# Optimization experiments

Measured on AMD Instinct MI355X. Metric: run time of the kernel, lower is better.

## Reference

```python
import jax, jax.numpy as jnp
import numpy as np

HEADS = 32
K_TOP = 512  # top-k tokens gathered from KV


def conv3d(x, w, b=None, pad=0, groups=1):
    # x: [B,C,D,H,W], w: [O, I/groups, kd,kh,kw]
    out = jax.lax.conv_general_dilated(
        x, w, window_strides=(1, 1, 1), padding=[(pad, pad)] * 3,
        dimension_numbers=("NCDHW", "OIDHW", "NCDHW"), feature_group_count=groups)
    if b is not None:
        out = out + b[None, :, None, None, None]
    return out


def setup_inputs() -> dict:
    key = jax.random.key(0)
    ks = jax.random.split(key, 10)
    B, C, D, H, W = 2, 256, 16, 16, 16
    p = lambda i, shape: (jax.random.normal(ks[i], shape, jnp.float32) * 0.02)
    return {
        "x_kv": jax.random.normal(ks[0], (B, C, D, H, W), jnp.float32),
        "x_q": jax.random.normal(ks[1], (B, C, D, H, W), jnp.float32),
        "w_spa": p(2, (1, 2, 7, 7, 7)),            # SpatialAttention conv, no bias
        "w_kv": p(3, (C, 2 * C)), "b_kv": jnp.zeros((2 * C,), jnp.float32),
        "w_q": p(4, (C, C)), "b_q": jnp.zeros((C,), jnp.float32),
        "w_proj": p(5, (C, C)), "b_proj": jnp.zeros((C,), jnp.float32),
        "w_dw": p(6, (C, 1, 3, 3, 3)), "b_dw": jnp.zeros((C,), jnp.float32),  # depthwise 3x3x3
        "w_pw": p(7, (C, C, 1, 1, 1)), "b_pw": jnp.zeros((C,), jnp.float32),  # pointwise 1x1x1
    }


def reference(x_kv, x_q, w_spa, w_kv, b_kv, w_q, b_q, w_proj, b_proj,
              w_dw, b_dw, w_pw, b_pw):
    B, C, D, H, W = x_kv.shape
    N = D * H * W
    hd = C // HEADS
    scale = hd ** -0.5

    # SpatialAttention: channel mean/max -> conv(2->1, k=7, pad=3) -> sigmoid
    avg = jnp.mean(x_kv, axis=1, keepdims=True)
    mx = jnp.max(x_kv, axis=1, keepdims=True)
    spa = jax.nn.sigmoid(conv3d(jnp.concatenate([avg, mx], axis=1), w_spa, None, pad=3))
    scores = spa.reshape(B, N)                      # [B, N]
    _, idx = jax.lax.top_k(scores, K_TOP)           # [B, K] (descending, like torch.topk)

    # Full K/V projection over all N tokens (as in original), then gather top-k
    xkv_t = x_kv.reshape(B, C, N).transpose(0, 2, 1)        # [B, N, C]
    kv = xkv_t @ w_kv + b_kv                                 # [B, N, 2C]
    k_full, v_full = kv[..., :C], kv[..., C:]
    k_g = jnp.take_along_axis(k_full, idx[:, :, None], axis=1)  # [B, K, C]
    v_g = jnp.take_along_axis(v_full, idx[:, :, None], axis=1)
    k_g = k_g.reshape(B, K_TOP, HEADS, hd).transpose(0, 2, 1, 3)  # [B, h, K, d]
    v_g = v_g.reshape(B, K_TOP, HEADS, hd).transpose(0, 2, 1, 3)

    # Queries over all Nq tokens
    xq_t = x_q.reshape(B, C, N).transpose(0, 2, 1)           # [B, N, C]
    q = (xq_t @ w_q + b_q).reshape(B, N, HEADS, hd).transpose(0, 2, 1, 3)  # [B, h, N, d]

    attn = jax.nn.softmax(jnp.einsum('bhnd,bhkd->bhnk', q, k_g) * scale, axis=-1)
    out = jnp.einsum('bhnk,bhkd->bhnd', attn, v_g)           # [B, h, N, d]
    out = out.transpose(0, 2, 1, 3).reshape(B, N, C)
    out = out @ w_proj + b_proj
    out = out.transpose(0, 2, 1).reshape(B, C, D, H, W)

    # DWconv residual on full (ungathered) V
    v_vol = v_full.transpose(0, 2, 1).reshape(B, C, D, H, W)
    res = conv3d(conv3d(v_vol, w_dw, b_dw, pad=1, groups=C), w_pw, b_pw)
    return out + res
```

## Files before the change

### kernel.cpp

```cpp
#include <hip/hip_runtime.h>
#include <hip/hip_bf16.h>

typedef short bf16x8 __attribute__((ext_vector_type(8)));
typedef float f32x4 __attribute__((ext_vector_type(4)));

constexpr int CN = 256, NV = 4096, KTOP = 512;

static __device__ __forceinline__ unsigned short f2bf(float f) {
  __hip_bfloat16 h = __float2bfloat16(f);
  return *(unsigned short*)&h;
}
static __device__ __forceinline__ unsigned pack2(float a, float b) {
  return (unsigned)f2bf(a) | ((unsigned)f2bf(b) << 16);
}
static __device__ __forceinline__ float bf2f(unsigned short u) {
  return __uint_as_float(((unsigned)u) << 16);
}
static __device__ __forceinline__ unsigned packtrunc(float a, float b) {
  return (__float_as_uint(a) >> 16) | (__float_as_uint(b) & 0xFFFF0000u);
}

__global__ void __launch_bounds__(256) k_stage1(const float* __restrict__ xkv,
                                                const float* __restrict__ xq,
                                                const float* __restrict__ wkv,
                                                const float* __restrict__ wq,
                                                const float* __restrict__ wproj,
                                                const float* __restrict__ wpw,
                                                unsigned short* __restrict__ xkv_t,
                                                unsigned short* __restrict__ xq_t,
                                                float* __restrict__ avgmx,
                                                unsigned short* __restrict__ wv_t,
                                                unsigned short* __restrict__ wq_t,
                                                unsigned short* __restrict__ wcat,
                                                unsigned short* __restrict__ wk_t) {
  __shared__ float tile[64 * 65];
  int z = blockIdx.z;
  int t = threadIdx.x;
  if (z == 4) {
    __shared__ float ssum[256], smax[256];
    int blk = blockIdx.y * 64 + blockIdx.x;
    int b = blk >> 7, n0 = (blk & 127) * 32;
    int cg = t >> 5, nl = t & 31;
    int n = n0 + nl;
    const float* p = xkv + (size_t)b * CN * NV + (size_t)cg * 32 * NV + n;
    float s = 0.f, m = -1e30f;
    for (int i = 0; i < 32; ++i) {
      float v = p[(size_t)i * NV];
      s += v; m = fmaxf(m, v);
    }
    ssum[t] = s; smax[t] = m;
    __syncthreads();
    if (cg == 0) {
      for (int g = 1; g < 8; ++g) { s += ssum[g * 32 + nl]; m = fmaxf(m, smax[g * 32 + nl]); }
      avgmx[(b * 2 + 0) * NV + n] = s * (1.0f / 256.0f);
      avgmx[(b * 2 + 1) * NV + n] = m;
    }
    return;
  }
  if (z >= 5) {
    if (blockIdx.x >= 4 || blockIdx.y >= 4) return;
    int role = z - 5;
    int j0 = blockIdx.x * 64, c0 = blockIdx.y * 64;
    if (role == 3) {
      int j = t >> 2, part = t & 3;
      const float* s = &wpw[(size_t)(j0 + j) * 256 + c0 + part * 16];
      unsigned w[8];
#pragma unroll
      for (int k = 0; k < 8; ++k) w[k] = pack2(s[2 * k], s[2 * k + 1]);
      uint4* p = (uint4*)&wcat[(size_t)(j0 + j) * 512 + 256 + c0 + part * 16];
      p[0] = make_uint4(w[0], w[1], w[2], w[3]);
      p[1] = make_uint4(w[4], w[5], w[6], w[7]);
      return;
    }
    const float* src; int srcLD, srcOff; unsigned short* dst; int dstLD;
    if (role == 0)      { src = wkv;   srcLD = 512; srcOff = 256; dst = wv_t; dstLD = 256; }
    else if (role == 1) { src = wq;    srcLD = 256; srcOff = 0;   dst = wq_t; dstLD = 256; }
    else if (role == 4) { src = wkv;   srcLD = 512; srcOff = 0;   dst = wk_t; dstLD = 256; }
    else                { src = wproj; srcLD = 256; srcOff = 0;   dst = wcat; dstLD = 512; }
    for (int i = 0; i < 16; ++i) {
      int id = i * 256 + t, c = id >> 6, j = id & 63;
      tile[c * 65 + j] = src[(size_t)(c0 + c) * srcLD + srcOff + j0 + j];
    }
    __syncthreads();
    int j = t & 63, part = t >> 6;
    unsigned w[8];
#pragma unroll
    for (int k = 0; k < 8; ++k)
      w[k] = pack2(tile[(part * 16 + 2 * k) * 65 + j], tile[(part * 16 + 2 * k + 1) * 65 + j]);
    uint4* p = (uint4*)&dst[(size_t)(j0 + j) * dstLD + c0 + part * 16];
    p[0] = make_uint4(w[0], w[1], w[2], w[3]);
    p[1] = make_uint4(w[4], w[5], w[6], w[7]);
    return;
  }
  int b = z & 1;
  const float* s = (z < 2 ? xkv : xq) + (size_t)b * CN * NV;
  unsigned short* d = (z < 2 ? xkv_t : xq_t) + (size_t)b * NV * 256;
  int c0 = blockIdx.y * 64, n0 = blockIdx.x * 64;
  for (int i = 0; i < 16; ++i) {
    int id = i * 256 + t, c = id >> 6, n = id & 63;
    tile[c * 65 + n] = s[(size_t)(c0 + c) * NV + n0 + n];
  }
  __syncthreads();
  int n = t & 63, part = t >> 6;
  unsigned w[8];
#pragma unroll
  for (int k = 0; k < 8; ++k)
    w[k] = pack2(tile[(part * 16 + 2 * k) * 65 + n], tile[(part * 16 + 2 * k + 1) * 65 + n]);
  uint4* p = (uint4*)&d[(size_t)(n0 + n) * 256 + c0 + part * 16];
  p[0] = make_uint4(w[0], w[1], w[2], w[3]);
  p[1] = make_uint4(w[4], w[5], w[6], w[7]);
}

__global__ void __launch_bounds__(256) k_stage2(const unsigned short* __restrict__ xkv_t,
                                                const unsigned short* __restrict__ xq_t,
                                                const unsigned short* __restrict__ wv_t,
                                                const unsigned short* __restrict__ wq_t,
                                                const float* __restrict__ bkv,
                                                const float* __restrict__ bq,
                                                const float* __restrict__ avgmx,
                                                const float* __restrict__ wspa,
                                                unsigned short* __restrict__ v_nc,
                                                unsigned short* __restrict__ qh,
                                                float* __restrict__ scores) {
  __shared__ alignas(16) char smem[35520];
  int z = blockIdx.z;
  int t = threadIdx.x;
  if (z == 4) {
    float* vol = (float*)smem;
    float* ws = (float*)(smem + 32768);
    int id = blockIdx.y * 32 + blockIdx.x;
    int b = id >> 5, chunk = id & 31;
    for (int i = t; i < 8192; i += 256) vol[i] = avgmx[b * 8192 + i];
    for (int i = t; i < 686; i += 256) ws[i] = wspa[i];
    __syncthreads();
    int ci = t & 1;
    int n = chunk * 128 + (t >> 1);
    int d = n >> 8, h = (n >> 4) & 15, w = n & 15;
    const float* vb = vol + ci * 4096;
    const float* wb = ws + ci * 343;
    float acc = 0.f;
    for (int kd = 0; kd < 7; ++kd) {
      int zd = d - 3 + kd; if ((unsigned)zd >= 16u) continue;
      for (int kh = 0; kh < 7; ++kh) {
        int zh = h - 3 + kh; if ((unsigned)zh >= 16u) continue;
        const float* row = vb + zd * 256 + zh * 16;
        const float* wr = wb + kd * 49 + kh * 7;
#pragma unroll
        for (int kw = 0; kw < 7; ++kw) {
          int zw = w - 3 + kw;
          if ((unsigned)zw < 16u) acc += row[zw] * wr[kw];
        }
      }
    }
    acc += __shfl_xor(acc, 1);
    if (ci == 0) scores[b * NV + n] = 1.0f / (1.0f + expf(-acc));
    return;
  }
  unsigned short* Als = (unsigned short*)smem;
  unsigned short* Bls = Als + 128 * 40;
  int role = z;
  int b = role & 1;
  bool isQ = role >= 2;
  const unsigned short* A = isQ ? wq_t : wv_t;
  const unsigned short* B = (isQ ? xq_t : xkv_t) + (size_t)b * NV * 256;
  const float* bias = isQ ? bq : (bkv + 256);
  int n0 = blockIdx.x * 128, j0 = blockIdx.y * 128;
  int wave = t >> 6, lane = t & 63;
  int l15 = lane & 15, q = lane >> 4, q8 = q * 8;
  int wj = (wave >> 1) * 64, wn = (wave & 1) * 64;
  f32x4 acc[4][4] = {};
  int ar = t >> 1, ah = t & 1;
  for (int c0 = 0; c0 < 256; c0 += 32) {
    __syncthreads();
    {
      const unsigned short* sa = &A[(size_t)(j0 + ar) * 256 + c0 + ah * 16];
      *(uint4*)&Als[ar * 40 + ah * 16]     = *(const uint4*)&sa[0];
      *(uint4*)&Als[ar * 40 + ah * 16 + 8] = *(const uint4*)&sa[8];
      const unsigned short* sb = &B[(size_t)(n0 + ar) * 256 + c0 + ah * 16];
      *(uint4*)&Bls[ar * 40 + ah * 16]     = *(const uint4*)&sb[0];
      *(uint4*)&Bls[ar * 40 + ah * 16 + 8] = *(const uint4*)&sb[8];
    }
    __syncthreads();
    bf16x8 af[4], bf[4];
#pragma unroll
    for (int mt = 0; mt < 4; ++mt)
      af[mt] = *(const bf16x8*)&Als[(wj + mt * 16 + l15) * 40 + q8];
#pragma unroll
    for (int nt = 0; nt < 4; ++nt)
      bf[nt] = *(const bf16x8*)&Bls[(wn + nt * 16 + l15) * 40 + q8];
#pragma unroll
    for (int mt = 0; mt < 4; ++mt)
#pragma unroll
      for (int nt = 0; nt < 4; ++nt)
        acc[mt][nt] = __builtin_amdgcn_mfma_f32_16x16x32_bf16(af[mt], bf[nt], acc[mt][nt], 0, 0, 0);
  }
#pragma unroll
  for (int mt = 0; mt < 4; ++mt) {
    int jb = j0 + wj + mt * 16 + q * 4;
    float4 b4 = *(const float4*)&bias[jb];
#pragma unroll
    for (int nt = 0; nt < 4; ++nt) {
      int n = n0 + wn + nt * 16 + l15;
      float v0 = acc[mt][nt][0] + b4.x;
      float v1 = acc[mt][nt][1] + b4.y;
      float v2 = acc[mt][nt][2] + b4.z;
      float v3 = acc[mt][nt][3] + b4.w;
      uint2 pk = make_uint2(pack2(v0, v1), pack2(v2, v3));
      if (isQ) {
        int h = jb >> 3, d0 = jb & 7;
        *(uint2*)&qh[((size_t)(b * 32 + h) * NV + n) * 8 + d0] = pk;
      } else {
        *(uint2*)&v_nc[((size_t)b * NV + n) * 256 + jb] = pk;
      }
    }
  }
}

__global__ void __launch_bounds__(1024) k_stage3(const float* __restrict__ scores,
                                                 int* __restrict__ idx,
                                                 const unsigned short* __restrict__ v_nc,
                                                 const float* __restrict__ wdw,
                                                 const float* __restrict__ bdw,
                                                 unsigned short* __restrict__ aoydw) {
  int b = blockIdx.z;
  int bx = blockIdx.x;
  int tid = threadIdx.x;
  if (bx == 256) {
    __shared__ unsigned sv[4096];
    __shared__ int sB;
    __shared__ unsigned sSub, scnt;
    __shared__ unsigned hist[256];
    __shared__ int wsum[16];
    for (int t = tid; t < 4096; t += 1024) sv[t] = __float_as_uint(scores[b * NV + t]);
    if (tid == 0) scnt = 0;
    unsigned prefix = 0;
    int r = 512;
    for (int shift = 24; shift >= 0; shift -= 8) {
      if (tid < 256) hist[tid] = 0;
      __syncthreads();
      unsigned maskhi = (shift == 24) ? 0u : (0xFFFFFFFFu << (shift + 8));
      for (int i = 0; i < 4; ++i) {
        unsigned v = sv[tid + i * 1024];
        if ((v & maskhi) == prefix) atomicAdd(&hist[(v >> shift) & 255], 1u);
      }
      __syncthreads();
      if (tid < 64) {
        int lane = tid;
        unsigned h0 = hist[lane * 4 + 0], h1 = hist[lane * 4 + 1];
        unsigned h2 = hist[lane * 4 + 2], h3 = hist[lane * 4 + 3];
        unsigned s = h0 + h1 + h2 + h3;
        for (int off = 1; off < 64; off <<= 1) {
          unsigned y = __shfl_down(s, off);
          if (lane + off < 64) s += y;
        }
        unsigned tail = __shfl_down(s, 1);
        if (lane == 63) tail = 0;
        unsigned s3 = tail + h3, s2 = s3 + h2, s1 = s2 + h1, s0 = s1 + h0;
        unsigned sx[5] = {s0, s1, s2, s3, tail};
#pragma unroll
        for (int i = 0; i < 4; ++i)
          if (sx[i] >= (unsigned)r && sx[i + 1] < (unsigned)r) { sB = lane * 4 + i; sSub = sx[i + 1]; }
      }
      __syncthreads();
      prefix |= ((unsigned)sB) << shift;
      r -= (int)sSub;
      __syncthreads();
    }
    unsigned vstar = prefix;
    for (int i = 0; i < 4; ++i) {
      int t = tid * 4 + i;
      if (sv[t] > vstar) { unsigned p = atomicAdd(&scnt, 1u); idx[b * KTOP + p] = t; }
    }
    __syncthreads();
    int base = (int)scnt;
    int loc = 0;
    for (int i = 0; i < 4; ++i) loc += (sv[tid * 4 + i] == vstar);
    int lane = tid & 63, w = tid >> 6;
    int x = loc;
    for (int off = 1; off < 64; off <<= 1) {
      int y = __shfl_up(x, off);
      if (lane >= off) x += y;
    }
    if (lane == 63) wsum[w] = x;
    __syncthreads();
    int wbase = 0;
    for (int i = 0; i < w; ++i) wbase += wsum[i];
    int excl = wbase + x - loc;
    for (int i = 0; i < 4; ++i) {
      int t = tid * 4 + i;
      if (sv[t] == vstar) {
        if (excl < r) idx[b * KTOP + base + excl] = t;
        ++excl;
      }
    }
    return;
  }
  int c = tid & 255;
  float wr[27];
#pragma unroll
  for (int i = 0; i < 27; ++i) wr[i] = wdw[c * 27 + i];
  float bias = bdw[c];
  const unsigned short* src = v_nc + (size_t)b * NV * 256 + c;
  unsigned short* dst = aoydw + (size_t)b * NV * 512 + 256 + c;
  int n = bx * 16 + (tid >> 8) * 4;
  int d = n >> 8, h = (n >> 4) & 15, w = n & 15;
  float a0 = bias, a1 = bias, a2 = bias, a3 = bias;
#pragma unroll
  for (int kd = 0; kd < 3; ++kd) {
    int zd = d - 1 + kd; bool okd = (unsigned)zd < 16u;
#pragma unroll
    for (int kh = 0; kh < 3; ++kh) {
      int zh = h - 1 + kh; bool okh = okd && ((unsigned)zh < 16u);
      int rowb = zd * 256 + zh * 16;
      float v[6];
#pragma unroll
      for (int i = 0; i < 6; ++i) {
        int zw = w - 1 + i;
        bool ok = okh && ((unsigned)zw < 16u);
        v[i] = ok ? bf2f(src[(size_t)(rowb + zw) * 256]) : 0.f;
      }
      const float* wp = &wr[kd * 9 + kh * 3];
      a0 = fmaf(v[0], wp[0], fmaf(v[1], wp[1], fmaf(v[2], wp[2], a0)));
      a1 = fmaf(v[1], wp[0], fmaf(v[2], wp[1], fmaf(v[3], wp[2], a1)));
      a2 = fmaf(v[2], wp[0], fmaf(v[3], wp[1], fmaf(v[4], wp[2], a2)));
      a3 = fmaf(v[3], wp[0], fmaf(v[4], wp[1], fmaf(v[5], wp[2], a3)));
    }
  }
  dst[(size_t)(n + 0) * 512] = f2bf(a0);
  dst[(size_t)(n + 1) * 512] = f2bf(a1);
  dst[(size_t)(n + 2) * 512] = f2bf(a2);
  dst[(size_t)(n + 3) * 512] = f2bf(a3);
}

__global__ void __launch_bounds__(256) k_kgvt(const unsigned short* __restrict__ xkv_t,
                                              const unsigned short* __restrict__ wk_t,
                                              const float* __restrict__ bkv,
                                              const int* __restrict__ map,
                                              const unsigned short* __restrict__ v_nc,
                                              unsigned short* __restrict__ kg,
                                              unsigned short* __restrict__ vt) {
  int b = blockIdx.z;
  int bx = blockIdx.x;
  int t = threadIdx.x;
  if (bx >= 128) {
    int h = bx - 128;
    int bh = b * 32 + h;
    unsigned short* dst = vt + (size_t)bh * 16 * 512;
    for (int i = t; i < 512; i += 256) dst[8 * 512 + i] = 0x3F80;
    for (int i = t; i < 512 * 7; i += 256) dst[9 * 512 + i] = 0;
    const int* ib = map + b * KTOP;
    for (int kk = t; kk < 512; kk += 256) {
      uint4 v = *(const uint4*)&v_nc[((size_t)b * NV + ib[kk]) * 256 + h * 8];
      unsigned short tmp[8];
      *(uint4*)tmp = v;
      int kc = kk >> 5, ka = kk & 31;
      int s = (ka < 16) ? ((ka >> 2) * 8 + (ka & 3))
                        : (((ka - 16) >> 2) * 8 + (ka & 3) + 4);
      int col = kc * 32 + s;
#pragma unroll
      for (int d = 0; d < 8; ++d) dst[d * 512 + col] = tmp[d];
    }
    return;
  }
  const float kscale = 0.35355339059327373f * 1.4426950408889634f;
  int wave = t >> 6, lane = t & 63;
  int l15 = lane & 15, quad = lane >> 4;
  int tile_id = bx * 4 + wave;
  int kt = tile_id & 31, jt = tile_id >> 5;
  int m0 = kt * 16, j0 = jt * 16;
  int nrow = map[b * KTOP + m0 + l15];
  const unsigned short* Arow = wk_t + (size_t)(j0 + l15) * 256 + quad * 8;
  const unsigned short* Brow = xkv_t + (size_t)b * NV * 256 + (size_t)nrow * 256 + quad * 8;
  f32x4 acc = {0.f, 0.f, 0.f, 0.f};
#pragma unroll
  for (int s = 0; s < 8; ++s) {
    bf16x8 af = *(const bf16x8*)&Arow[s * 32];
    bf16x8 bf = *(const bf16x8*)&Brow[s * 32];
    acc = __builtin_amdgcn_mfma_f32_16x16x32_bf16(af, bf, acc, 0, 0, 0);
  }
  int h = (j0 >> 3) + (quad >> 1), d0b = (quad & 1) * 4;
  int jb = j0 + quad * 4;
  float4 b4 = *(const float4*)&bkv[jb];
  int m = m0 + l15;
  float v0 = (acc[0] + b4.x) * kscale;
  float v1 = (acc[1] + b4.y) * kscale;
  float v2 = (acc[2] + b4.z) * kscale;
  float v3 = (acc[3] + b4.w) * kscale;
  *(uint2*)&kg[((size_t)(b * 32 + h) * KTOP + m) * 8 + d0b] =
      make_uint2(pack2(v0, v1), pack2(v2, v3));
}

__global__ void __launch_bounds__(256) k_fattn(const unsigned short* __restrict__ qh,
                                               const unsigned short* __restrict__ kg,
                                               const unsigned short* __restrict__ vt,
                                               unsigned short* __restrict__ aoydw) {
  int bh = blockIdx.x;
  int b = bh >> 5, h = bh & 31;
  int t = threadIdx.x, wave = t >> 6, lane = t & 63;
  int l15 = lane & 15, quad = lane >> 4;
  int n0 = blockIdx.y * 128 + wave * 32;
  bf16x8 q0 = {}, q1 = {};
  if (quad == 0) {
    q0 = *(const bf16x8*)&qh[((size_t)bh * NV + n0 + l15) * 8];
    q1 = *(const bf16x8*)&qh[((size_t)bh * NV + n0 + 16 + l15) * 8];
  }
  const unsigned short* kbase = kg + (size_t)bh * KTOP * 8;
  const unsigned short* vbase = vt + (size_t)bh * 16 * 512;
  f32x4 acc0 = {0.f, 0.f, 0.f, 0.f}, acc1 = {0.f, 0.f, 0.f, 0.f};
  bf16x8 kA0 = {}, kA1 = {};
  if (quad == 0) {
    kA0 = *(const bf16x8*)&kbase[(size_t)l15 * 8];
    kA1 = *(const bf16x8*)&kbase[(size_t)(16 + l15) * 8];
  }
  for (int kc = 0; kc < 16; ++kc) {
    bf16x8 nA0 = {}, nA1 = {};
    if (quad == 0 && kc < 15) {
      nA0 = *(const bf16x8*)&kbase[(size_t)(kc * 32 + 32 + l15) * 8];
      nA1 = *(const bf16x8*)&kbase[(size_t)(kc * 32 + 48 + l15) * 8];
    }
    bf16x8 bV = *(const bf16x8*)&vbase[(size_t)l15 * 512 + kc * 32 + quad * 8];
    f32x4 z = {0.f, 0.f, 0.f, 0.f};
    f32x4 s00 = __builtin_amdgcn_mfma_f32_16x16x32_bf16(kA0, q0, z, 0, 0, 0);
    f32x4 s01 = __builtin_amdgcn_mfma_f32_16x16x32_bf16(kA1, q0, z, 0, 0, 0);
    f32x4 s10 = __builtin_amdgcn_mfma_f32_16x16x32_bf16(kA0, q1, z, 0, 0, 0);
    f32x4 s11 = __builtin_amdgcn_mfma_f32_16x16x32_bf16(kA1, q1, z, 0, 0, 0);
    uint4 P0, P1;
    P0.x = packtrunc(__builtin_amdgcn_exp2f(s00[0]), __builtin_amdgcn_exp2f(s00[1]));
    P0.y = packtrunc(__builtin_amdgcn_exp2f(s00[2]), __builtin_amdgcn_exp2f(s00[3]));
    P0.z = packtrunc(__builtin_amdgcn_exp2f(s01[0]), __builtin_amdgcn_exp2f(s01[1]));
    P0.w = packtrunc(__builtin_amdgcn_exp2f(s01[2]), __builtin_amdgcn_exp2f(s01[3]));
    P1.x = packtrunc(__builtin_amdgcn_exp2f(s10[0]), __builtin_amdgcn_exp2f(s10[1]));
    P1.y = packtrunc(__builtin_amdgcn_exp2f(s10[2]), __builtin_amdgcn_exp2f(s10[3]));
    P1.z = packtrunc(__builtin_amdgcn_exp2f(s11[0]), __builtin_amdgcn_exp2f(s11[1]));
    P1.w = packtrunc(__builtin_amdgcn_exp2f(s11[2]), __builtin_amdgcn_exp2f(s11[3]));
    acc0 = __builtin_amdgcn_mfma_f32_16x16x32_bf16(*(bf16x8*)&P0, bV, acc0, 0, 0, 0);
    acc1 = __builtin_amdgcn_mfma_f32_16x16x32_bf16(*(bf16x8*)&P1, bV, acc1, 0, 0, 0);
    kA0 = nA0; kA1 = nA1;
  }
#pragma unroll
  for (int tq = 0; tq < 2; ++tq) {
    f32x4 a = tq ? acc1 : acc0;
#pragma unroll
    for (int r = 0; r < 4; ++r) {
      float se = __shfl(a[r], quad * 16 + 8);
      float o = a[r] * (1.0f / se);
      if (l15 < 8) {
        int n = n0 + tq * 16 + quad * 4 + r;
        aoydw[((size_t)b * NV + n) * 512 + h * 8 + l15] = f2bf(o);
      }
    }
  }
}

__global__ void __launch_bounds__(256) k_final(const unsigned short* __restrict__ aoydw,
                                               const unsigned short* __restrict__ wcat,
                                               const float* __restrict__ bproj,
                                               const float* __restrict__ bpw,
                                               float* __restrict__ out) {
  __shared__ unsigned short Als[64 * 40];
  __shared__ unsigned short Bls[128 * 40];
  int n0 = blockIdx.x * 64, j0 = blockIdx.y * 128, b = blockIdx.z;
  int t = threadIdx.x;
  int wave = t >> 6, lane = t & 63;
  int l15 = lane & 15, q = lane >> 4, q8 = q * 8;
  int wn = (wave >> 1) * 32, wjj = (wave & 1) * 64;
  f32x4 acc[2][4] = {};
  const unsigned short* Abase = aoydw + (size_t)b * NV * 512;
  int ar = t >> 2, aq = t & 3;
  int br = t >> 1, bhh = t & 1;
  for (int c0 = 0; c0 < 512; c0 += 32) {
    __syncthreads();
    *(uint4*)&Als[ar * 40 + aq * 8] =
        *(const uint4*)&Abase[(size_t)(n0 + ar) * 512 + c0 + aq * 8];
    const unsigned short* sb = &wcat[(size_t)(j0 + br) * 512 + c0 + bhh * 16];
    *(uint4*)&Bls[br * 40 + bhh * 16]     = *(const uint4*)&sb[0];
    *(uint4*)&Bls[br * 40 + bhh * 16 + 8] = *(const uint4*)&sb[8];
    __syncthreads();
    bf16x8 af[2], bf[4];
#pragma unroll
    for (int mt = 0; mt < 2; ++mt)
      af[mt] = *(const bf16x8*)&Als[(wn + mt * 16 + l15) * 40 + q8];
#pragma unroll
    for (int nt = 0; nt < 4; ++nt)
      bf[nt] = *(const bf16x8*)&Bls[(wjj + nt * 16 + l15) * 40 + q8];
#pragma unroll
    for (int mt = 0; mt < 2; ++mt)
#pragma unroll
      for (int nt = 0; nt < 4; ++nt)
        acc[mt][nt] = __builtin_amdgcn_mfma_f32_16x16x32_bf16(af[mt], bf[nt], acc[mt][nt], 0, 0, 0);
  }
#pragma unroll
  for (int nt = 0; nt < 4; ++nt) {
    int j = j0 + wjj + nt * 16 + l15;
    float bl = bproj[j] + bpw[j];
#pragma unroll
    for (int mt = 0; mt < 2; ++mt) {
      int n = n0 + wn + mt * 16 + q * 4;
      float4 r = make_float4(acc[mt][nt][0] + bl, acc[mt][nt][1] + bl,
                             acc[mt][nt][2] + bl, acc[mt][nt][3] + bl);
      *(float4*)&out[(size_t)(b * 256 + j) * NV + n] = r;
    }
  }
}

extern "C" void kernel_launch(void* const* d_in, const int* in_sizes, int n_in,
                              void* d_out, int out_size, void* d_ws, size_t ws_size,
                              hipStream_t stream) {
  const float* x_kv   = (const float*)d_in[0];
  const float* x_q    = (const float*)d_in[1];
  const float* w_spa  = (const float*)d_in[2];
  const float* w_kv   = (const float*)d_in[3];
  const float* b_kv   = (const float*)d_in[4];
  const float* w_q    = (const float*)d_in[5];
  const float* b_q    = (const float*)d_in[6];
  const float* w_proj = (const float*)d_in[7];
  const float* b_proj = (const float*)d_in[8];
  const float* w_dw   = (const float*)d_in[9];
  const float* b_dw   = (const float*)d_in[10];
  const float* w_pw   = (const float*)d_in[11];
  const float* b_pw   = (const float*)d_in[12];
  float* out = (float*)d_out;

  const size_t MB = 1024 * 1024;
  char* ws = (char*)d_ws;
  unsigned short* xkv_t = (unsigned short*)(ws);
  unsigned short* xq_t  = (unsigned short*)(ws + 4 * MB);
  unsigned short* v_nc  = (unsigned short*)(ws + 8 * MB);
  unsigned short* qh    = (unsigned short*)(ws + 12 * MB);
  unsigned short* aoydw = (unsigned short*)(ws + 16 * MB);
  unsigned short* kg    = (unsigned short*)(ws + 24 * MB);
  unsigned short* vt    = (unsigned short*)(ws + 24 * MB + 512 * 1024);
  unsigned short* wv_t  = (unsigned short*)(ws + 26 * MB);
  unsigned short* wq_t  = (unsigned short*)(ws + 26 * MB + 131072);
  unsigned short* wcat  = (unsigned short*)(ws + 26 * MB + 262144);
  unsigned short* wk_t  = (unsigned short*)(ws + 26 * MB + 524288);
  float*          avgmx = (float*)(ws + 27 * MB);
  float*          scores= (float*)(ws + 27 * MB + 65536);
  int*            idx   = (int*)  (ws + 27 * MB + 98304);

  k_stage1<<<dim3(64, 4, 10), 256, 0, stream>>>(x_kv, x_q, w_kv, w_q, w_proj, w_pw,
                                                xkv_t, xq_t, avgmx, wv_t, wq_t, wcat, wk_t);
  k_stage2<<<dim3(32, 2, 5), 256, 0, stream>>>(xkv_t, xq_t, wv_t, wq_t, b_kv, b_q,
                                               avgmx, w_spa, v_nc, qh, scores);
  k_stage3<<<dim3(257, 1, 2), 1024, 0, stream>>>(scores, idx, v_nc, w_dw, b_dw, aoydw);
  k_kgvt<<<dim3(160, 1, 2), 256, 0, stream>>>(xkv_t, wk_t, b_kv, idx, v_nc, kg, vt);
  k_fattn<<<dim3(64, 32), 256, 0, stream>>>(qh, kg, vt, aoydw);
  k_final<<<dim3(64, 2, 2), 256, 0, stream>>>(aoydw, wcat, b_proj, b_pw, out);
}
```

Measured before the change: 188.1 us.

## Shrink GEMM tiles for more blocks and vectorize stage-1 loads

The stage-2 projection GEMM output tile drops from 128x128 to 64x128, and the final GEMM tile drops from 64x128 to 64x64 with a 64-wide K step. Both changes double the grid size to improve occupancy and CU coverage on this small problem. Stage-1 channel mean/max and the transpose tile loads now use float4 vector loads, with the mean/max reduction handled by fewer blocks. Smaller tiles cost more redundant global loads per output, and the final kernel's larger K step changes how it uses shared memory.

```diff
diff --git a/kernel.cpp b/kernel.cpp
--- a/kernel.cpp
+++ b/kernel.cpp
@@ -33,27 +33,38 @@
                                                 unsigned short* __restrict__ wq_t,
                                                 unsigned short* __restrict__ wcat,
                                                 unsigned short* __restrict__ wk_t) {
-  __shared__ float tile[64 * 65];
+  __shared__ float tile[64 * 68];
   int z = blockIdx.z;
   int t = threadIdx.x;
   if (z == 4) {
-    __shared__ float ssum[256], smax[256];
+    __shared__ float4 ssum4[256], smax4[256];
     int blk = blockIdx.y * 64 + blockIdx.x;
-    int b = blk >> 7, n0 = (blk & 127) * 32;
+    if (blk >= 64) return;
+    int b = blk >> 5, n0r = (blk & 31) * 128;
     int cg = t >> 5, nl = t & 31;
-    int n = n0 + nl;
+    int n = n0r + nl * 4;
     const float* p = xkv + (size_t)b * CN * NV + (size_t)cg * 32 * NV + n;
-    float s = 0.f, m = -1e30f;
+    float4 s4 = make_float4(0.f, 0.f, 0.f, 0.f);
+    float4 m4 = make_float4(-1e30f, -1e30f, -1e30f, -1e30f);
     for (int i = 0; i < 32; ++i) {
-      float v = p[(size_t)i * NV];
-      s += v; m = fmaxf(m, v);
-    }
-    ssum[t] = s; smax[t] = m;
+      float4 v = *(const float4*)&p[(size_t)i * NV];
+      s4.x += v.x; s4.y += v.y; s4.z += v.z; s4.w += v.w;
+      m4.x = fmaxf(m4.x, v.x); m4.y = fmaxf(m4.y, v.y);
+      m4.z = fmaxf(m4.z, v.z); m4.w = fmaxf(m4.w, v.w);
+    }
+    ssum4[t] = s4; smax4[t] = m4;
     __syncthreads();
     if (cg == 0) {
-      for (int g = 1; g < 8; ++g) { s += ssum[g * 32 + nl]; m = fmaxf(m, smax[g * 32 + nl]); }
-      avgmx[(b * 2 + 0) * NV + n] = s * (1.0f / 256.0f);
-      avgmx[(b * 2 + 1) * NV + n] = m;
+      for (int g = 1; g < 8; ++g) {
+        float4 o = ssum4[g * 32 + nl], x = smax4[g * 32 + nl];
+        s4.x += o.x; s4.y += o.y; s4.z += o.z; s4.w += o.w;
+        m4.x = fmaxf(m4.x, x.x); m4.y = fmaxf(m4.y, x.y);
+        m4.z = fmaxf(m4.z, x.z); m4.w = fmaxf(m4.w, x.w);
+      }
+      float4 a4 = make_float4(s4.x * (1.0f / 256.0f), s4.y * (1.0f / 256.0f),
+                              s4.z * (1.0f / 256.0f), s4.w * (1.0f / 256.0f));
+      *(float4*)&avgmx[(size_t)(b * 2 + 0) * NV + n] = a4;
+      *(float4*)&avgmx[(size_t)(b * 2 + 1) * NV + n] = m4;
     }
     return;
   }
@@ -96,16 +107,17 @@
   const float* s = (z < 2 ? xkv : xq) + (size_t)b * CN * NV;
   unsigned short* d = (z < 2 ? xkv_t : xq_t) + (size_t)b * NV * 256;
   int c0 = blockIdx.y * 64, n0 = blockIdx.x * 64;
-  for (int i = 0; i < 16; ++i) {
-    int id = i * 256 + t, c = id >> 6, n = id & 63;
-    tile[c * 65 + n] = s[(size_t)(c0 + c) * NV + n0 + n];
+#pragma unroll
+  for (int i = 0; i < 4; ++i) {
+    int id = i * 256 + t, c = id >> 4, nq = (id & 15) * 4;
+    *(float4*)&tile[c * 68 + nq] = *(const float4*)&s[(size_t)(c0 + c) * NV + n0 + nq];
   }
   __syncthreads();
   int n = t & 63, part = t >> 6;
   unsigned w[8];
 #pragma unroll
   for (int k = 0; k < 8; ++k)
-    w[k] = pack2(tile[(part * 16 + 2 * k) * 65 + n], tile[(part * 16 + 2 * k + 1) * 65 + n]);
+    w[k] = pack2(tile[(part * 16 + 2 * k) * 68 + n], tile[(part * 16 + 2 * k + 1) * 68 + n]);
   uint4* p = (uint4*)&d[(size_t)(n0 + n) * 256 + c0 + part * 16];
   p[0] = make_uint4(w[0], w[1], w[2], w[3]);
   p[1] = make_uint4(w[4], w[5], w[6], w[7]);
@@ -126,9 +138,10 @@
   int z = blockIdx.z;
   int t = threadIdx.x;
   if (z == 4) {
+    int id = blockIdx.y * 32 + blockIdx.x;
+    if (id >= 64) return;
     float* vol = (float*)smem;
     float* ws = (float*)(smem + 32768);
-    int id = blockIdx.y * 32 + blockIdx.x;
     int b = id >> 5, chunk = id & 31;
     for (int i = t; i < 8192; i += 256) vol[i] = avgmx[b * 8192 + i];
     for (int i = t; i < 686; i += 256) ws[i] = wspa[i];
@@ -157,45 +170,43 @@
     return;
   }
   unsigned short* Als = (unsigned short*)smem;
-  unsigned short* Bls = Als + 128 * 40;
+  unsigned short* Bls = Als + 64 * 40;
   int role = z;
   int b = role & 1;
   bool isQ = role >= 2;
   const unsigned short* A = isQ ? wq_t : wv_t;
   const unsigned short* B = (isQ ? xq_t : xkv_t) + (size_t)b * NV * 256;
   const float* bias = isQ ? bq : (bkv + 256);
-  int n0 = blockIdx.x * 128, j0 = blockIdx.y * 128;
+  int n0 = blockIdx.x * 128, j0 = blockIdx.y * 64;
   int wave = t >> 6, lane = t & 63;
   int l15 = lane & 15, q = lane >> 4, q8 = q * 8;
-  int wj = (wave >> 1) * 64, wn = (wave & 1) * 64;
-  f32x4 acc[4][4] = {};
-  int ar = t >> 1, ah = t & 1;
+  int wj = (wave >> 1) * 32, wn = (wave & 1) * 64;
+  f32x4 acc[2][4] = {};
+  int arA = t >> 2, ahA = t & 3;
+  int brB = t >> 1, bhB = t & 1;
   for (int c0 = 0; c0 < 256; c0 += 32) {
     __syncthreads();
-    {
-      const unsigned short* sa = &A[(size_t)(j0 + ar) * 256 + c0 + ah * 16];
-      *(uint4*)&Als[ar * 40 + ah * 16]     = *(const uint4*)&sa[0];
-      *(uint4*)&Als[ar * 40 + ah * 16 + 8] = *(const uint4*)&sa[8];
-      const unsigned short* sb = &B[(size_t)(n0 + ar) * 256 + c0 + ah * 16];
-      *(uint4*)&Bls[ar * 40 + ah * 16]     = *(const uint4*)&sb[0];
-      *(uint4*)&Bls[ar * 40 + ah * 16 + 8] = *(const uint4*)&sb[8];
-    }
-    __syncthreads();
-    bf16x8 af[4], bf[4];
-#pragma unroll
-    for (int mt = 0; mt < 4; ++mt)
+    *(uint4*)&Als[arA * 40 + ahA * 8] =
+        *(const uint4*)&A[(size_t)(j0 + arA) * 256 + c0 + ahA * 8];
+    const unsigned short* sb = &B[(size_t)(n0 + brB) * 256 + c0 + bhB * 16];
+    *(uint4*)&Bls[brB * 40 + bhB * 16]     = *(const uint4*)&sb[0];
+    *(uint4*)&Bls[brB * 40 + bhB * 16 + 8] = *(const uint4*)&sb[8];
+    __syncthreads();
+    bf16x8 af[2], bf[4];
+#pragma unroll
+    for (int mt = 0; mt < 2; ++mt)
       af[mt] = *(const bf16x8*)&Als[(wj + mt * 16 + l15) * 40 + q8];
 #pragma unroll
     for (int nt = 0; nt < 4; ++nt)
       bf[nt] = *(const bf16x8*)&Bls[(wn + nt * 16 + l15) * 40 + q8];
 #pragma unroll
-    for (int mt = 0; mt < 4; ++mt)
+    for (int mt = 0; mt < 2; ++mt)
 #pragma unroll
       for (int nt = 0; nt < 4; ++nt)
         acc[mt][nt] = __builtin_amdgcn_mfma_f32_16x16x32_bf16(af[mt], bf[nt], acc[mt][nt], 0, 0, 0);
   }
 #pragma unroll
-  for (int mt = 0; mt < 4; ++mt) {
+  for (int mt = 0; mt < 2; ++mt) {
     int jb = j0 + wj + mt * 16 + q * 4;
     float4 b4 = *(const float4*)&bias[jb];
 #pragma unroll
@@ -457,40 +468,45 @@
                                                const float* __restrict__ bproj,
                                                const float* __restrict__ bpw,
                                                float* __restrict__ out) {
-  __shared__ unsigned short Als[64 * 40];
-  __shared__ unsigned short Bls[128 * 40];
-  int n0 = blockIdx.x * 64, j0 = blockIdx.y * 128, b = blockIdx.z;
+  __shared__ unsigned short Als[64 * 72];
+  __shared__ unsigned short Bls[64 * 72];
+  int n0 = blockIdx.x * 64, j0 = blockIdx.y * 64, b = blockIdx.z;
   int t = threadIdx.x;
   int wave = t >> 6, lane = t & 63;
   int l15 = lane & 15, q = lane >> 4, q8 = q * 8;
-  int wn = (wave >> 1) * 32, wjj = (wave & 1) * 64;
-  f32x4 acc[2][4] = {};
+  int wn = (wave & 1) * 32, wjj = (wave >> 1) * 32;
+  f32x4 acc[2][2] = {};
   const unsigned short* Abase = aoydw + (size_t)b * NV * 512;
   int ar = t >> 2, aq = t & 3;
-  int br = t >> 1, bhh = t & 1;
-  for (int c0 = 0; c0 < 512; c0 += 32) {
-    __syncthreads();
-    *(uint4*)&Als[ar * 40 + aq * 8] =
+  for (int c0 = 0; c0 < 512; c0 += 64) {
+    __syncthreads();
+    *(uint4*)&Als[ar * 72 + aq * 8] =
         *(const uint4*)&Abase[(size_t)(n0 + ar) * 512 + c0 + aq * 8];
-    const unsigned short* sb = &wcat[(size_t)(j0 + br) * 512 + c0 + bhh * 16];
-    *(uint4*)&Bls[br * 40 + bhh * 16]     = *(const uint4*)&sb[0];
-    *(uint4*)&Bls[br * 40 + bhh * 16 + 8] = *(const uint4*)&sb[8];
-    __syncthreads();
-    bf16x8 af[2], bf[4];
-#pragma unroll
-    for (int mt = 0; mt < 2; ++mt)
-      af[mt] = *(const bf16x8*)&Als[(wn + mt * 16 + l15) * 40 + q8];
-#pragma unroll
-    for (int nt = 0; nt < 4; ++nt)
-      bf[nt] = *(const bf16x8*)&Bls[(wjj + nt * 16 + l15) * 40 + q8];
-#pragma unroll
-    for (int mt = 0; mt < 2; ++mt)
-#pragma unroll
-      for (int nt = 0; nt < 4; ++nt)
-        acc[mt][nt] = __builtin_amdgcn_mfma_f32_16x16x32_bf16(af[mt], bf[nt], acc[mt][nt], 0, 0, 0);
-  }
-#pragma unroll
-  for (int nt = 0; nt < 4; ++nt) {
+    *(uint4*)&Als[ar * 72 + 32 + aq * 8] =
+        *(const uint4*)&Abase[(size_t)(n0 + ar) * 512 + c0 + 32 + aq * 8];
+    *(uint4*)&Bls[ar * 72 + aq * 8] =
+        *(const uint4*)&wcat[(size_t)(j0 + ar) * 512 + c0 + aq * 8];
+    *(uint4*)&Bls[ar * 72 + 32 + aq * 8] =
+        *(const uint4*)&wcat[(size_t)(j0 + ar) * 512 + c0 + 32 + aq * 8];
+    __syncthreads();
+#pragma unroll
+    for (int kk = 0; kk < 2; ++kk) {
+      bf16x8 af[2], bf[2];
+#pragma unroll
+      for (int mt = 0; mt < 2; ++mt)
+        af[mt] = *(const bf16x8*)&Als[(wn + mt * 16 + l15) * 72 + kk * 32 + q8];
+#pragma unroll
+      for (int nt = 0; nt < 2; ++nt)
+        bf[nt] = *(const bf16x8*)&Bls[(wjj + nt * 16 + l15) * 72 + kk * 32 + q8];
+#pragma unroll
+      for (int mt = 0; mt < 2; ++mt)
+#pragma unroll
+        for (int nt = 0; nt < 2; ++nt)
+          acc[mt][nt] = __builtin_amdgcn_mfma_f32_16x16x32_bf16(af[mt], bf[nt], acc[mt][nt], 0, 0, 0);
+    }
+  }
+#pragma unroll
+  for (int nt = 0; nt < 2; ++nt) {
     int j = j0 + wjj + nt * 16 + l15;
     float bl = bproj[j] + bpw[j];
 #pragma unroll
@@ -540,10 +556,10 @@
 
   k_stage1<<<dim3(64, 4, 10), 256, 0, stream>>>(x_kv, x_q, w_kv, w_q, w_proj, w_pw,
                                                 xkv_t, xq_t, avgmx, wv_t, wq_t, wcat, wk_t);
-  k_stage2<<<dim3(32, 2, 5), 256, 0, stream>>>(xkv_t, xq_t, wv_t, wq_t, b_kv, b_q,
+  k_stage2<<<dim3(32, 4, 5), 256, 0, stream>>>(xkv_t, xq_t, wv_t, wq_t, b_kv, b_q,
                                                avgmx, w_spa, v_nc, qh, scores);
   k_stage3<<<dim3(257, 1, 2), 1024, 0, stream>>>(scores, idx, v_nc, w_dw, b_dw, aoydw);
   k_kgvt<<<dim3(160, 1, 2), 256, 0, stream>>>(xkv_t, wk_t, b_kv, idx, v_nc, kg, vt);
   k_fattn<<<dim3(64, 32), 256, 0, stream>>>(qh, kg, vt, aoydw);
-  k_final<<<dim3(64, 2, 2), 256, 0, stream>>>(aoydw, wcat, b_proj, b_pw, out);
-}
+  k_final<<<dim3(64, 4, 2), 256, 0, stream>>>(aoydw, wcat, b_proj, b_pw, out);
+}
```

Result: faster. 182.4 us (-3.0%).
